# Kernel optimization log

Measured on AMD Instinct MI355X. Metric: run time of the kernel, lower is better.

Reference implementation:

```python
import jax, jax.numpy as jnp
import numpy as np

B, T, ENC_DIM, DEC_DIM = 64, 2048, 1024, 1024


def setup_inputs() -> dict:
    key = jax.random.key(0)
    k1, k2, k3, k4, k5 = jax.random.split(key, 5)
    enc_out = jax.random.normal(k1, (B, T, ENC_DIM), dtype=jnp.float32)
    dec_state = jax.random.normal(k2, (B, DEC_DIM), dtype=jnp.float32)
    # nn.Linear(enc_dim+dec_dim, dec_dim): weight [dec_dim, enc_dim+dec_dim], bias [dec_dim]
    fan_in = ENC_DIM + DEC_DIM
    bound = 1.0 / np.sqrt(fan_in)
    W_weight = jax.random.uniform(k3, (DEC_DIM, fan_in), minval=-bound, maxval=bound, dtype=jnp.float32)
    W_bias = jax.random.uniform(k4, (DEC_DIM,), minval=-bound, maxval=bound, dtype=jnp.float32)
    # nn.Linear(dec_dim, 1, bias=False): weight [1, dec_dim]
    bound_v = 1.0 / np.sqrt(DEC_DIM)
    v_weight = jax.random.uniform(k5, (1, DEC_DIM), minval=-bound_v, maxval=bound_v, dtype=jnp.float32)
    return {"enc_out": enc_out, "dec_state": dec_state, "W_weight": W_weight, "W_bias": W_bias, "v_weight": v_weight}


def reference(enc_out, dec_state, W_weight, W_bias, v_weight):
    enc_dim = enc_out.shape[-1]
    # split W over the concat axis: cat([enc_out, dec_state]) @ W.T == enc_out @ We.T + dec_state @ Wd.T
    We = W_weight[:, :enc_dim]   # [dec_dim, enc_dim]
    Wd = W_weight[:, enc_dim:]   # [dec_dim, dec_dim]
    # [B,T,dec_dim] + [B,1,dec_dim] broadcast (avoids repeat/concat materialization)
    energy = jnp.tanh(
        jnp.einsum('bte,de->btd', enc_out, We)
        + (jnp.einsum('bd,ed->be', dec_state, Wd) + W_bias)[:, None, :]
    )
    scores = jnp.einsum('btd,d->bt', energy, v_weight[0])  # [B,T]
    alpha = jax.nn.softmax(scores, axis=1)
    context = jnp.einsum('bte,bt->be', enc_out, alpha)     # [B,enc_dim]
    return context
```

## Files before the change

kernel.cpp:

```cpp
#include <hip/hip_runtime.h>
#include <hip/hip_bf16.h>
#include <cmath>

#define BB 64
#define TT 2048
#define EE 1024
#define DD 1024
#define FAN 2048

typedef __attribute__((ext_vector_type(8))) short bhalf8;
typedef __attribute__((ext_vector_type(4))) float fvec4;

#define OFF_WE   0u
#define OFF_C    2097152u
#define OFF_SP   2359296u
#define OFF_A    4456448u
#define OFF_P    4980736u
#define OFF_ENCB 8388608u
#define WS_NEED  (OFF_ENCB + (size_t)BB * TT * EE * 2)

__device__ __forceinline__ short f2bf(float f) {
    unsigned int u = __float_as_uint(f);
    u += 0x7FFFu + ((u >> 16) & 1u);
    return (short)(u >> 16);
}

__device__ __forceinline__ bhalf8 cvt8(float4 a, float4 b) {
    bhalf8 h;
    h[0] = f2bf(a.x); h[1] = f2bf(a.y); h[2] = f2bf(a.z); h[3] = f2bf(a.w);
    h[4] = f2bf(b.x); h[5] = f2bf(b.y); h[6] = f2bf(b.z); h[7] = f2bf(b.w);
    return h;
}

__device__ __forceinline__ float fast_tanhf(float x) {
    float ax = __builtin_fabsf(x);
    float e  = __expf(-2.0f * ax);
    float r  = (1.0f - e) * __builtin_amdgcn_rcpf(1.0f + e);
    return __builtin_copysignf(r, x);
}

__device__ __forceinline__ void dma16(const void* g, void* l) {
    __builtin_amdgcn_global_load_lds(
        (const __attribute__((address_space(1))) void*)g,
        (__attribute__((address_space(3))) void*)l,
        16, 0, 0);
}

__global__ void prep_we_k(const float* __restrict__ W, short* __restrict__ wsWe) {
    int g  = blockIdx.x * 256 + threadIdx.x;
    int ec = g >> 12;
    int eo = (g >> 10) & 3;
    int d  = g & 1023;
    const float* src = W + (size_t)d * FAN + ec * 32 + eo * 8;
    float4 f0 = *(const float4*)src;
    float4 f1 = *(const float4*)(src + 4);
    *(bhalf8*)((char*)wsWe + (size_t)ec * 65536 + eo * 16384 + d * 16) = cvt8(f0, f1);
}

__global__ void prep_c_k(const float* __restrict__ W, const float* __restrict__ bias,
                         const float* __restrict__ dec, float* __restrict__ cbuf) {
    int wg   = blockIdx.x * 4 + (threadIdx.x >> 6);
    int lane = threadIdx.x & 63;
    int b = wg >> 10, d = wg & 1023;
    const float* wrow = W + (size_t)d * FAN + EE;
    const float* drow = dec + b * DD;
    float p = 0.f;
#pragma unroll
    for (int i = 0; i < 16; ++i)
        p += wrow[i * 64 + lane] * drow[i * 64 + lane];
#pragma unroll
    for (int off = 1; off < 64; off <<= 1)
        p += __shfl_xor(p, off);
    if (lane == 0) cbuf[b * DD + d] = p + bias[d];
}

__global__ void prep_encb_k(const float* __restrict__ enc, short* __restrict__ encB) {
    size_t g = (size_t)blockIdx.x * 256 + threadIdx.x;
    const float* src = enc + g * 8;
    float4 f0 = *(const float4*)src;
    float4 f1 = *(const float4*)(src + 4);
    *(bhalf8*)(encB + g * 8) = cvt8(f0, f1);
}

__global__ __launch_bounds__(512, 4)
void scores_k(const short* __restrict__ encB, const short* __restrict__ wsWe,
              const float* __restrict__ cbuf, const float* __restrict__ vw,
              float* __restrict__ sp) {
    __shared__ __align__(16) short smA[3][8192];
    __shared__ float sRed[8][64];

    const int tid  = threadIdx.x;
    const int w    = tid >> 6;
    const int wm   = w >> 2;
    const int wn   = w & 3;
    const int lane = tid & 63;
    const int lrow = lane >> 4;
    const int lcol = lane & 15;
    const int b  = blockIdx.y;
    const int tt = blockIdx.x >> 2;
    const int dq = blockIdx.x & 3;
    const int t0 = tt * 128;

    const int tJ = tid >> 3;
    const int xg = (tid & 7) ^ (tJ & 7);
    const char* gA = (const char*)encB + ((size_t)(b * TT + t0 + tJ)) * 2048 + xg * 16;

    const char* Bbase = (const char*)wsWe + lrow * 16384
                      + (size_t)(dq * 256 + wn * 64 + lcol) * 16;

    fvec4 acc[4][4];
#pragma unroll
    for (int m = 0; m < 4; ++m)
#pragma unroll
        for (int n = 0; n < 4; ++n)
            acc[m][n] = (fvec4){0.f, 0.f, 0.f, 0.f};

    const int ax0 = ((lrow)     ^ (lcol & 7)) * 16;
    const int ax1 = ((4 + lrow) ^ (lcol & 7)) * 16;
    const int tb0 = (wm * 64 + lcol) * 128;

    bhalf8 bfA[4], bfB[4];

#define DMA_TILE(K, S)                                                        \
    do {                                                                      \
        dma16(gA + (size_t)(K) * 128,          (char*)smA[(S)] + tid * 16);   \
        dma16(gA + 131072 + (size_t)(K) * 128, (char*)smA[(S)] + tid * 16 + 8192); \
    } while (0)

    DMA_TILE(0, 0);
    DMA_TILE(1, 1);
#pragma unroll
    for (int n = 0; n < 4; ++n)
        bfA[n] = *(const bhalf8*)(Bbase + n * 256);
    asm volatile("s_waitcnt vmcnt(6)" ::: "memory");
    __builtin_amdgcn_s_barrier();

#define STEP(I, S, SS, DOSTAGE, DOPRE)                                        \
    do {                                                                      \
        if (DOSTAGE) DMA_TILE((I) + 2, SS);                                   \
                                                                     \
        {                                                                     \
            _Pragma("unroll")                                                 \
            for (int n = 0; n < 4; ++n)                                       \
                bfB[n] = *(const bhalf8*)(Bbase                               \
                          + (size_t)(2 * (I) + 1) * 65536 + n * 256);         \
            bhalf8 af[4];                                                     \
            _Pragma("unroll")                                                 \
            for (int m = 0; m < 4; ++m)                                       \
                af[m] = *(const bhalf8*)((const char*)smA[(S)]                \
                          + tb0 + m * 2048 + ax0);                            \
            __builtin_amdgcn_s_setprio(1);                                    \
            _Pragma("unroll")                                                 \
            for (int n = 0; n < 4; ++n)                                       \
                _Pragma("unroll")                                             \
                for (int m = 0; m < 4; ++m)                                   \
                    acc[m][n] = __builtin_amdgcn_mfma_f32_16x16x32_bf16(      \
                        af[m], bfA[n], acc[m][n], 0, 0, 0);                   \
            __builtin_amdgcn_s_setprio(0);                                    \
        }                                                                     \
                                                                     \
        {                                                                     \
            if (DOPRE) {                                                      \
                _Pragma("unroll")                                             \
                for (int n = 0; n < 4; ++n)                                   \
                    bfA[n] = *(const bhalf8*)(Bbase                           \
                              + (size_t)(2 * (I) + 2) * 65536 + n * 256);     \
            }                                                                 \
            bhalf8 af[4];                                                     \
            _Pragma("unroll")                                                 \
            for (int m = 0; m < 4; ++m)                                       \
                af[m] = *(const bhalf8*)((const char*)smA[(S)]                \
                          + tb0 + m * 2048 + ax1);                            \
            __builtin_amdgcn_s_setprio(1);                                    \
            _Pragma("unroll")                                                 \
            for (int n = 0; n < 4; ++n)                                       \
                _Pragma("unroll")                                             \
                for (int m = 0; m < 4; ++m)                                   \
                    acc[m][n] = __builtin_amdgcn_mfma_f32_16x16x32_bf16(      \
                        af[m], bfB[n], acc[m][n], 0, 0, 0);                   \
            __builtin_amdgcn_s_setprio(0);                                    \
        }                                                                     \
    } while (0)

#define WB(N)                                                                 \
    do {                                                                      \
        asm volatile("s_waitcnt vmcnt(" #N ")" ::: "memory");                 \
        __builtin_amdgcn_s_barrier();                                         \
    } while (0)

    STEP(0, 0, 2, 1, 1);  WB(6);
    STEP(1, 1, 0, 1, 1);  WB(6);
    STEP(2, 2, 1, 1, 1);  WB(6);
    STEP(3, 0, 2, 1, 1);  WB(6);
    STEP(4, 1, 0, 1, 1);  WB(6);
    STEP(5, 2, 1, 1, 1);  WB(6);
    STEP(6, 0, 2, 1, 1);  WB(6);
    STEP(7, 1, 0, 1, 1);  WB(6);
    STEP(8, 2, 1, 1, 1);  WB(6);
    STEP(9, 0, 2, 1, 1);  WB(6);
    STEP(10, 1, 0, 1, 1); WB(6);
    STEP(11, 2, 1, 1, 1); WB(6);
    STEP(12, 0, 2, 1, 1); WB(6);
    STEP(13, 1, 0, 1, 1); WB(6);
    STEP(14, 2, 0, 0, 1); WB(4);
    STEP(15, 0, 0, 0, 0);
#undef STEP
#undef WB
#undef DMA_TILE

    float cv[4], vv[4];
#pragma unroll
    for (int n = 0; n < 4; ++n) {
        int d = dq * 256 + wn * 64 + n * 16 + lcol;
        cv[n] = cbuf[b * DD + d];
        vv[n] = vw[d];
    }

#pragma unroll
    for (int m = 0; m < 4; ++m) {
#pragma unroll
        for (int j = 0; j < 4; ++j) {
            float p = 0.f;
#pragma unroll
            for (int n = 0; n < 4; ++n)
                p += vv[n] * fast_tanhf(acc[m][n][j] + cv[n]);
            p += __shfl_xor(p, 1); p += __shfl_xor(p, 2);
            p += __shfl_xor(p, 4); p += __shfl_xor(p, 8);
            if (lcol == 0) sRed[w][m * 16 + lrow * 4 + j] = p;
        }
    }
    __syncthreads();
    if (tid < 128) {
        int r  = tid;
        int rm = r >> 6, lr = r & 63;
        float v2 = sRed[rm * 4 + 0][lr] + sRed[rm * 4 + 1][lr]
                 + sRed[rm * 4 + 2][lr] + sRed[rm * 4 + 3][lr];
        sp[((size_t)dq * BB + b) * TT + t0 + r] = v2;
    }
}

__global__ __launch_bounds__(512, 4)
void scores_fb_k(const float* __restrict__ enc, const short* __restrict__ wsWe,
                 const float* __restrict__ cbuf, const float* __restrict__ vw,
                 float* __restrict__ sp) {
    __shared__ short sA[2][4][128][8];
    __shared__ float sRed[8][64];
    const int tid  = threadIdx.x;
    const int w    = tid >> 6;
    const int wm   = w >> 2;
    const int wn   = w & 3;
    const int lane = tid & 63;
    const int lrow = lane >> 4;
    const int lcol = lane & 15;
    const int b  = blockIdx.y;
    const int tt = blockIdx.x >> 2;
    const int dq = blockIdx.x & 3;
    const int t0 = tt * 128;
    const int st  = tid >> 2;
    const int seo = tid & 3;
    const int stw = st ^ (seo << 2);
    const float* gsrc = enc + ((size_t)(b * TT + t0 + st)) * EE + seo * 8;
    fvec4 acc[4][4];
#pragma unroll
    for (int m = 0; m < 4; ++m)
#pragma unroll
        for (int n = 0; n < 4; ++n)
            acc[m][n] = (fvec4){0.f, 0.f, 0.f, 0.f};
    const char* Bbase = (const char*)wsWe + lrow * 16384
                      + (size_t)(dq * 256 + wn * 64 + lcol) * 16;
    {
        float4 x0 = *(const float4*)(gsrc);
        float4 x1 = *(const float4*)(gsrc + 4);
        *(bhalf8*)&sA[0][seo][stw][0] = cvt8(x0, x1);
    }
    __syncthreads();
#pragma unroll 2
    for (int i = 0; i < 32; ++i) {
        const int buf = i & 1;
        float4 x0, x1;
        if (i < 31) {
            x0 = *(const float4*)(gsrc + (i + 1) * 32);
            x1 = *(const float4*)(gsrc + (i + 1) * 32 + 4);
        }
        bhalf8 bf[4];
#pragma unroll
        for (int n = 0; n < 4; ++n)
            bf[n] = *(const bhalf8*)(Bbase + (size_t)i * 65536 + n * 256);
        bhalf8 af[4];
#pragma unroll
        for (int m = 0; m < 4; ++m) {
            int t = wm * 64 + m * 16 + lcol;
            af[m] = *(const bhalf8*)&sA[buf][lrow][t ^ (lrow << 2)][0];
        }
#pragma unroll
        for (int n = 0; n < 4; ++n)
#pragma unroll
            for (int m = 0; m < 4; ++m)
                acc[m][n] = __builtin_amdgcn_mfma_f32_16x16x32_bf16(af[m], bf[n], acc[m][n], 0, 0, 0);
        if (i < 31)
            *(bhalf8*)&sA[buf ^ 1][seo][stw][0] = cvt8(x0, x1);
        __syncthreads();
    }
    float cv[4], vv[4];
#pragma unroll
    for (int n = 0; n < 4; ++n) {
        int d = dq * 256 + wn * 64 + n * 16 + lcol;
        cv[n] = cbuf[b * DD + d];
        vv[n] = vw[d];
    }
#pragma unroll
    for (int m = 0; m < 4; ++m) {
#pragma unroll
        for (int j = 0; j < 4; ++j) {
            float p = 0.f;
#pragma unroll
            for (int n = 0; n < 4; ++n)
                p += vv[n] * fast_tanhf(acc[m][n][j] + cv[n]);
            p += __shfl_xor(p, 1); p += __shfl_xor(p, 2);
            p += __shfl_xor(p, 4); p += __shfl_xor(p, 8);
            if (lcol == 0) sRed[w][m * 16 + lrow * 4 + j] = p;
        }
    }
    __syncthreads();
    if (tid < 128) {
        int r  = tid;
        int rm = r >> 6, lr = r & 63;
        float v2 = sRed[rm * 4 + 0][lr] + sRed[rm * 4 + 1][lr]
                 + sRed[rm * 4 + 2][lr] + sRed[rm * 4 + 3][lr];
        sp[((size_t)dq * BB + b) * TT + t0 + r] = v2;
    }
}

__global__ void softmax_k(const float* __restrict__ sp, float* __restrict__ alpha) {
    int b = blockIdx.x, tid = threadIdx.x;
    float s[8];
    float m = -1e30f;
#pragma unroll
    for (int i = 0; i < 8; ++i) {
        size_t idx = (size_t)b * TT + i * 256 + tid;
        s[i] = sp[idx] + sp[(size_t)BB * TT + idx]
             + sp[2 * (size_t)BB * TT + idx] + sp[3 * (size_t)BB * TT + idx];
        m = fmaxf(m, s[i]);
    }
#pragma unroll
    for (int off = 1; off < 64; off <<= 1) m = fmaxf(m, __shfl_xor(m, off));
    __shared__ float red[4], red2[4];
    if ((tid & 63) == 0) red[tid >> 6] = m;
    __syncthreads();
    m = fmaxf(fmaxf(red[0], red[1]), fmaxf(red[2], red[3]));
    float sum = 0.f;
#pragma unroll
    for (int i = 0; i < 8; ++i) { s[i] = expf(s[i] - m); sum += s[i]; }
#pragma unroll
    for (int off = 1; off < 64; off <<= 1) sum += __shfl_xor(sum, off);
    if ((tid & 63) == 0) red2[tid >> 6] = sum;
    __syncthreads();
    sum = red2[0] + red2[1] + red2[2] + red2[3];
    float inv = 1.0f / sum;
#pragma unroll
    for (int i = 0; i < 8; ++i) alpha[b * TT + i * 256 + tid] = s[i] * inv;
}

__global__ void ctx_k(const float* __restrict__ enc, const float* __restrict__ alpha,
                      float* __restrict__ part) {
    int ts = blockIdx.x, b = blockIdx.y, tid = threadIdx.x;
    __shared__ float sAl[256];
    sAl[tid] = alpha[b * TT + ts * 256 + tid];
    __syncthreads();
    float4 acc = {0.f, 0.f, 0.f, 0.f};
    const float* base = enc + ((size_t)b * TT + ts * 256) * EE + tid * 4;
#pragma unroll 8
    for (int i = 0; i < 256; ++i) {
        float4 v = *(const float4*)(base + (size_t)i * EE);
        float a = sAl[i];
        acc.x += a * v.x; acc.y += a * v.y; acc.z += a * v.z; acc.w += a * v.w;
    }
    *(float4*)&part[(size_t)(ts * 64 + b) * EE + tid * 4] = acc;
}

__global__ void comb_k(const float* __restrict__ part, float* __restrict__ out) {
    int g = blockIdx.x * 256 + threadIdx.x;
    float s = 0.f;
#pragma unroll
    for (int ts = 0; ts < 8; ++ts) s += part[(size_t)ts * 65536 + g];
    out[g] = s;
}

extern "C" void kernel_launch(void* const* d_in, const int* in_sizes, int n_in,
                              void* d_out, int out_size, void* d_ws, size_t ws_size,
                              hipStream_t stream) {
    const float* enc  = (const float*)d_in[0];
    const float* dec  = (const float*)d_in[1];
    const float* W    = (const float*)d_in[2];
    const float* bias = (const float*)d_in[3];
    const float* vw   = (const float*)d_in[4];
    float* out = (float*)d_out;

    char* ws = (char*)d_ws;
    short* wsWe   = (short*)(ws + OFF_WE);
    float* cbuf   = (float*)(ws + OFF_C);
    float* sp     = (float*)(ws + OFF_SP);
    float* alpha  = (float*)(ws + OFF_A);
    float* part   = (float*)(ws + OFF_P);
    short* encB   = (short*)(ws + OFF_ENCB);

    prep_we_k<<<512, 256, 0, stream>>>(W, wsWe);
    prep_c_k<<<16384, 256, 0, stream>>>(W, bias, dec, cbuf);
    if (ws_size >= WS_NEED) {
        prep_encb_k<<<65536, 256, 0, stream>>>(enc, encB);
        scores_k<<<dim3(64, 64), 512, 0, stream>>>(encB, wsWe, cbuf, vw, sp);
    } else {
        scores_fb_k<<<dim3(64, 64), 512, 0, stream>>>(enc, wsWe, cbuf, vw, sp);
    }
    softmax_k<<<64, 256, 0, stream>>>(sp, alpha);
    ctx_k<<<dim3(8, 64), 256, 0, stream>>>(enc, alpha, part);
    comb_k<<<256, 256, 0, stream>>>(part, out);
}
```

Before: 532.1 us.

## Read bf16 encoder copy in context pass and tile decoder-bias GEMV

The context kernel now reads the bf16 copy of enc_out that already exists for the scores GEMM, instead of the fp32 original. This halves that pass's global traffic. It also splits T into 16 chunks of 128 with 128-thread blocks, so the combine step sums 16 partials and the partial buffer is enlarged. The prep_c kernel is rewritten as a shared-memory tiled GEMV over 64 blocks instead of one wave per output. The trade-off is bf16 rounding in the context sum, which lowers accuracy.

```diff
diff --git a/kernel.cpp b/kernel.cpp
--- a/kernel.cpp
+++ b/kernel.cpp
@@ -16,13 +16,18 @@
 #define OFF_SP   2359296u
 #define OFF_A    4456448u
 #define OFF_P    4980736u
-#define OFF_ENCB 8388608u
+#define OFF_ENCB 16777216u
 #define WS_NEED  (OFF_ENCB + (size_t)BB * TT * EE * 2)
 
 __device__ __forceinline__ short f2bf(float f) {
     unsigned int u = __float_as_uint(f);
     u += 0x7FFFu + ((u >> 16) & 1u);
     return (short)(u >> 16);
+}
+
+__device__ __forceinline__ float bf2f(short s) {
+    unsigned int u = ((unsigned int)(unsigned short)s) << 16;
+    return __uint_as_float(u);
 }
 
 __device__ __forceinline__ bhalf8 cvt8(float4 a, float4 b) {
@@ -57,21 +62,48 @@
     *(bhalf8*)((char*)wsWe + (size_t)ec * 65536 + eo * 16384 + d * 16) = cvt8(f0, f1);
 }
 
-__global__ void prep_c_k(const float* __restrict__ W, const float* __restrict__ bias,
-                         const float* __restrict__ dec, float* __restrict__ cbuf) {
-    int wg   = blockIdx.x * 4 + (threadIdx.x >> 6);
-    int lane = threadIdx.x & 63;
-    int b = wg >> 10, d = wg & 1023;
-    const float* wrow = W + (size_t)d * FAN + EE;
-    const float* drow = dec + b * DD;
-    float p = 0.f;
-#pragma unroll
-    for (int i = 0; i < 16; ++i)
-        p += wrow[i * 64 + lane] * drow[i * 64 + lane];
-#pragma unroll
-    for (int off = 1; off < 64; off <<= 1)
-        p += __shfl_xor(p, off);
-    if (lane == 0) cbuf[b * DD + d] = p + bias[d];
+__global__ __launch_bounds__(256)
+void prep_c_k(const float* __restrict__ W, const float* __restrict__ bias,
+              const float* __restrict__ dec, float* __restrict__ cbuf) {
+    __shared__ float wd[16][68];
+    __shared__ float dc[64][68];
+    const int tid = threadIdx.x;
+    const int d0  = blockIdx.x * 16;
+    const int b   = tid >> 2;
+    const int dg  = tid & 3;
+    float acc[4] = {0.f, 0.f, 0.f, 0.f};
+    const int r  = tid >> 2;
+    const int c4 = (tid & 3) * 16;
+    for (int ec = 0; ec < 16; ++ec) {
+        if (tid < 64) {
+            const float* ws = W + (size_t)(d0 + r) * FAN + EE + ec * 64 + c4;
+#pragma unroll
+            for (int q = 0; q < 4; ++q)
+                *(float4*)&wd[r][c4 + q * 4] = *(const float4*)(ws + q * 4);
+        }
+        {
+            const float* ds = dec + (size_t)r * DD + ec * 64 + c4;
+#pragma unroll
+            for (int q = 0; q < 4; ++q)
+                *(float4*)&dc[r][c4 + q * 4] = *(const float4*)(ds + q * 4);
+        }
+        __syncthreads();
+#pragma unroll 4
+        for (int e = 0; e < 64; e += 4) {
+            float4 dv = *(const float4*)&dc[b][e];
+#pragma unroll
+            for (int i = 0; i < 4; ++i) {
+                float4 wv = *(const float4*)&wd[dg * 4 + i][e];
+                acc[i] += wv.x * dv.x + wv.y * dv.y + wv.z * dv.z + wv.w * dv.w;
+            }
+        }
+        __syncthreads();
+    }
+#pragma unroll
+    for (int i = 0; i < 4; ++i) {
+        int d = d0 + dg * 4 + i;
+        cbuf[b * DD + d] = acc[i] + bias[d];
+    }
 }
 
 __global__ void prep_encb_k(const float* __restrict__ enc, short* __restrict__ encB) {
@@ -138,7 +170,6 @@
 #define STEP(I, S, SS, DOSTAGE, DOPRE)                                        \
     do {                                                                      \
         if (DOSTAGE) DMA_TILE((I) + 2, SS);                                   \
-                                                                     \
         {                                                                     \
             _Pragma("unroll")                                                 \
             for (int n = 0; n < 4; ++n)                                       \
@@ -158,7 +189,6 @@
                         af[m], bfA[n], acc[m][n], 0, 0, 0);                   \
             __builtin_amdgcn_s_setprio(0);                                    \
         }                                                                     \
-                                                                     \
         {                                                                     \
             if (DOPRE) {                                                      \
                 _Pragma("unroll")                                             \
@@ -361,28 +391,53 @@
     for (int i = 0; i < 8; ++i) alpha[b * TT + i * 256 + tid] = s[i] * inv;
 }
 
-__global__ void ctx_k(const float* __restrict__ enc, const float* __restrict__ alpha,
+__global__ void ctx_k(const short* __restrict__ encB, const float* __restrict__ alpha,
                       float* __restrict__ part) {
     int ts = blockIdx.x, b = blockIdx.y, tid = threadIdx.x;
-    __shared__ float sAl[256];
-    sAl[tid] = alpha[b * TT + ts * 256 + tid];
-    __syncthreads();
-    float4 acc = {0.f, 0.f, 0.f, 0.f};
-    const float* base = enc + ((size_t)b * TT + ts * 256) * EE + tid * 4;
+    __shared__ float sAl[128];
+    sAl[tid] = alpha[b * TT + ts * 128 + tid];
+    __syncthreads();
+    float acc[8] = {0.f, 0.f, 0.f, 0.f, 0.f, 0.f, 0.f, 0.f};
+    const short* base = encB + ((size_t)(b * TT + ts * 128)) * EE + tid * 8;
 #pragma unroll 8
-    for (int i = 0; i < 256; ++i) {
-        float4 v = *(const float4*)(base + (size_t)i * EE);
+    for (int i = 0; i < 128; ++i) {
+        bhalf8 v = *(const bhalf8*)(base + (size_t)i * EE);
         float a = sAl[i];
-        acc.x += a * v.x; acc.y += a * v.y; acc.z += a * v.z; acc.w += a * v.w;
-    }
-    *(float4*)&part[(size_t)(ts * 64 + b) * EE + tid * 4] = acc;
+#pragma unroll
+        for (int j = 0; j < 8; ++j)
+            acc[j] += a * bf2f(v[j]);
+    }
+    float* dst = &part[((size_t)(ts * 64 + b)) * EE + tid * 8];
+    *(float4*)dst       = (float4){acc[0], acc[1], acc[2], acc[3]};
+    *(float4*)(dst + 4) = (float4){acc[4], acc[5], acc[6], acc[7]};
+}
+
+__global__ void ctx_fb_k(const float* __restrict__ enc, const float* __restrict__ alpha,
+                         float* __restrict__ part) {
+    int ts = blockIdx.x, b = blockIdx.y, tid = threadIdx.x;
+    __shared__ float sAl[128];
+    sAl[tid] = alpha[b * TT + ts * 128 + tid];
+    __syncthreads();
+    float4 a0 = {0.f, 0.f, 0.f, 0.f}, a1 = {0.f, 0.f, 0.f, 0.f};
+    const float* base = enc + ((size_t)(b * TT + ts * 128)) * EE + tid * 8;
+#pragma unroll 8
+    for (int i = 0; i < 128; ++i) {
+        float4 v0 = *(const float4*)(base + (size_t)i * EE);
+        float4 v1 = *(const float4*)(base + (size_t)i * EE + 4);
+        float a = sAl[i];
+        a0.x += a * v0.x; a0.y += a * v0.y; a0.z += a * v0.z; a0.w += a * v0.w;
+        a1.x += a * v1.x; a1.y += a * v1.y; a1.z += a * v1.z; a1.w += a * v1.w;
+    }
+    float* dst = &part[((size_t)(ts * 64 + b)) * EE + tid * 8];
+    *(float4*)dst = a0;
+    *(float4*)(dst + 4) = a1;
 }
 
 __global__ void comb_k(const float* __restrict__ part, float* __restrict__ out) {
     int g = blockIdx.x * 256 + threadIdx.x;
     float s = 0.f;
 #pragma unroll
-    for (int ts = 0; ts < 8; ++ts) s += part[(size_t)ts * 65536 + g];
+    for (int ts = 0; ts < 16; ++ts) s += part[(size_t)ts * 65536 + g];
     out[g] = s;
 }
 
@@ -405,14 +460,16 @@
     short* encB   = (short*)(ws + OFF_ENCB);
 
     prep_we_k<<<512, 256, 0, stream>>>(W, wsWe);
-    prep_c_k<<<16384, 256, 0, stream>>>(W, bias, dec, cbuf);
+    prep_c_k<<<64, 256, 0, stream>>>(W, bias, dec, cbuf);
     if (ws_size >= WS_NEED) {
         prep_encb_k<<<65536, 256, 0, stream>>>(enc, encB);
         scores_k<<<dim3(64, 64), 512, 0, stream>>>(encB, wsWe, cbuf, vw, sp);
+        softmax_k<<<64, 256, 0, stream>>>(sp, alpha);
+        ctx_k<<<dim3(16, 64), 128, 0, stream>>>(encB, alpha, part);
     } else {
         scores_fb_k<<<dim3(64, 64), 512, 0, stream>>>(enc, wsWe, cbuf, vw, sp);
-    }
-    softmax_k<<<64, 256, 0, stream>>>(sp, alpha);
-    ctx_k<<<dim3(8, 64), 256, 0, stream>>>(enc, alpha, part);
+        softmax_k<<<64, 256, 0, stream>>>(sp, alpha);
+        ctx_fb_k<<<dim3(16, 64), 128, 0, stream>>>(enc, alpha, part);
+    }
     comb_k<<<256, 256, 0, stream>>>(part, out);
 }
```

Measured after the change: 514.5 us. 1.03x faster.
